# Performance work log

Hardware: AMD Instinct MI355X
Metric: run time of the kernel (lower is better)

The kernel has to match this reference:

```python
import jax, jax.numpy as jnp
import numpy as np

EMBED_DIM = 512
NUM_HEADS = 8
NUM_RULES = 16
HEAD_DIM = EMBED_DIM // NUM_HEADS


def setup_inputs() -> dict:
    key = jax.random.key(0)
    ks = jax.random.split(key, 10)
    B, S, E, H, R, D = 4, 2048, EMBED_DIM, NUM_HEADS, NUM_RULES, HEAD_DIM
    lim_q = 1.0 / np.sqrt(E)
    lim_v = 1.0 / np.sqrt(E)
    return {
        "query": jax.random.normal(ks[0], (B, S, E), jnp.float32),
        "key": jax.random.normal(ks[1], (B, S, E), jnp.float32),
        "value": jax.random.normal(ks[2], (B, S, E), jnp.float32),
        "Wq": jax.random.uniform(ks[3], (E, E), jnp.float32, -lim_q, lim_q),
        "bq": jax.random.uniform(ks[4], (E,), jnp.float32, -lim_q, lim_q),
        "Wv": jax.random.uniform(ks[5], (E * R, E), jnp.float32, -lim_v, lim_v),
        "bv": jax.random.uniform(ks[6], (E * R,), jnp.float32, -lim_v, lim_v),
        "Wo": jax.random.uniform(ks[7], (E, E), jnp.float32, -lim_q, lim_q),
        "bo": jax.random.uniform(ks[8], (E,), jnp.float32, -lim_q, lim_q),
        "rules_keys": 0.02 * jax.random.normal(ks[9], (H, R, D), jnp.float32),
        "rules_widths": jnp.ones((H, R, D), jnp.float32),
    }


def reference(query, key, value, Wq, bq, Wv, bv, Wo, bo, rules_keys, rules_widths):
    B, S, E = query.shape
    H, R, D = NUM_HEADS, NUM_RULES, HEAD_DIM
    scale = D ** -0.5
    # preprocessing_query: Linear + scale, split heads -> (b, h, s, d)
    q = (query @ Wq.T + bq) * scale
    q = q.reshape(B, S, H, D).transpose(0, 2, 1, 3)
    # custom_distance (l1): |q - rule_key| broadcast over rules -> (b, h, s, r, d)
    diff = jnp.abs(q[:, :, :, None, :] - rules_keys[None, :, None, :, :])
    # get_z_values: z = mean_d( -0.5 * (diff / width)^2 ) -> (b, h, s, r)
    z = -0.5 * jnp.mean(jnp.square(diff / rules_widths[None, :, None, :, :]), axis=-1)
    # softmax over rules (last dim), dropout is identity (p=0)
    attn = jax.nn.softmax(z, axis=-1)  # (b, h, s, r)
    # preprocessing_value: Linear(E -> E*R) + scale, 'b s (h d r) -> b s h d r'
    v = (value @ Wv.T + bv) * scale
    v = v.reshape(B, S, H, D, R)
    # Fnn_output = attn * v summed over rules -> (b, s, h, d)
    out = jnp.einsum("bhsr,bshdr->bshd", attn, v)
    # torch: (b,s,h,d).transpose(1,2).contiguous().view(b, -1, h*d)
    out = out.transpose(0, 2, 1, 3).reshape(B, -1, H * D)
    return out @ Wo.T + bo
```

## Files before the change

kernel.cpp:

```cpp
#include <hip/hip_runtime.h>
#include <stdint.h>

#define TOKENS 8192
#define EDIM 512
#define HNUM 8
#define RNUM 16
#define DDIM 64
#define KDIM 512

typedef short v8s __attribute__((ext_vector_type(8)));
typedef float v4f __attribute__((ext_vector_type(4)));

__device__ inline float b2f(unsigned short u) {
    union { unsigned int i; float f; } c; c.i = ((unsigned int)u) << 16; return c.f;
}
__device__ inline unsigned short f2b(float f) {
    union { float f; unsigned int i; } c; c.f = f;
    unsigned int i = c.i + 0x7fffu + ((c.i >> 16) & 1u);
    return (unsigned short)(i >> 16);
}

#define GLD16(dst, src) \
    __builtin_amdgcn_global_load_lds((__attribute__((address_space(1))) void*)(src), \
                                     (__attribute__((address_space(3))) void*)(dst), 16, 0, 0)

__global__ __launch_bounds__(256)
void cvt5(const float* __restrict__ s0, const float* __restrict__ s1,
          const float* __restrict__ s2, const float* __restrict__ s3,
          const float* __restrict__ s4,
          unsigned short* __restrict__ d0, unsigned short* __restrict__ d1,
          unsigned short* __restrict__ d2, unsigned short* __restrict__ d3,
          unsigned short* __restrict__ d4,
          int n0, int n1, int n2, int n3, int n4)
{
    const float* s; unsigned short* d; int n;
    switch (blockIdx.y) {
        case 0: s = s0; d = d0; n = n0; break;
        case 1: s = s1; d = d1; n = n1; break;
        case 2: s = s2; d = d2; n = n2; break;
        case 3: s = s3; d = d3; n = n3; break;
        default: s = s4; d = d4; n = n4; break;
    }
    size_t base = (size_t)blockIdx.x * 2048 + (size_t)threadIdx.x * 8;
    if (base >= (size_t)n) return;
    const float4* sp = (const float4*)(s + base);
    float4 f0 = sp[0], f1 = sp[1];
    v8s o;
    o[0] = (short)f2b(f0.x); o[1] = (short)f2b(f0.y);
    o[2] = (short)f2b(f0.z); o[3] = (short)f2b(f0.w);
    o[4] = (short)f2b(f1.x); o[5] = (short)f2b(f1.y);
    o[6] = (short)f2b(f1.z); o[7] = (short)f2b(f1.w);
    *(v8s*)(d + base) = o;
}

template <int MODE>
__global__ __launch_bounds__(256, 4)
void gemm64(const unsigned short* __restrict__ A,
            const unsigned short* __restrict__ B,
            const float* __restrict__ bias,
            float* __restrict__ outF,
            unsigned short* __restrict__ outH)
{
    __shared__ unsigned short As[64 * 32];
    __shared__ unsigned short Bs[64 * 32];

    const int tid  = threadIdx.x;
    const int w    = tid >> 6;
    const int lane = tid & 63;
    const int quad = lane >> 4;
    const int l16  = lane & 15;
    const int wm   = w >> 1, wn = w & 1;
    const int m0   = blockIdx.x * 64;
    const int n0   = blockIdx.y * 64;

    v4f acc[2][2];
#pragma unroll
    for (int i = 0; i < 2; ++i)
#pragma unroll
        for (int j = 0; j < 2; ++j)
            acc[i][j] = (v4f){0.f, 0.f, 0.f, 0.f};

    for (int kt = 0; kt < KDIM / 32; ++kt) {
        int c = w * 64 + lane;
        const unsigned short* sa = A + (size_t)(m0 + (c >> 2)) * KDIM + kt * 32 + (c & 3) * 8;
        GLD16(&As[w * 512], sa);
        const unsigned short* sb = B + (size_t)(n0 + (c >> 2)) * KDIM + kt * 32 + (c & 3) * 8;
        GLD16(&Bs[w * 512], sb);
        __syncthreads();

        v8s af[2], bf[2];
#pragma unroll
        for (int mt = 0; mt < 2; ++mt)
            af[mt] = *(const v8s*)&As[(wm * 32 + mt * 16 + l16) * 32 + quad * 8];
#pragma unroll
        for (int nt = 0; nt < 2; ++nt)
            bf[nt] = *(const v8s*)&Bs[(wn * 32 + nt * 16 + l16) * 32 + quad * 8];
#pragma unroll
        for (int mt = 0; mt < 2; ++mt)
#pragma unroll
            for (int nt = 0; nt < 2; ++nt)
                acc[mt][nt] = __builtin_amdgcn_mfma_f32_16x16x32_bf16(af[mt], bf[nt], acc[mt][nt], 0, 0, 0);
        __syncthreads();
    }

#pragma unroll
    for (int mt = 0; mt < 2; ++mt)
#pragma unroll
        for (int nt = 0; nt < 2; ++nt) {
            int col = n0 + wn * 32 + nt * 16 + l16;
            float bb = bias[col];
#pragma unroll
            for (int rg = 0; rg < 4; ++rg) {
                int row = m0 + wm * 32 + mt * 16 + quad * 4 + rg;
                float v = acc[mt][nt][rg] + bb;
                if (MODE == 0) outH[(size_t)row * EDIM + col] = f2b(v * 0.125f);
                else           outF[(size_t)row * EDIM + col] = v;
            }
        }
}

__device__ __forceinline__ v8s ldfrag(const unsigned short* base, int r, int g) {
    return *(const v8s*)(base + (r << 6) + ((g ^ (r & 7)) << 3));
}

#define BAR   __builtin_amdgcn_s_barrier()
#define LGKM0 asm volatile("s_waitcnt lgkmcnt(0)" ::: "memory")
#define WAITV(n) asm volatile("s_waitcnt vmcnt(" #n ")" ::: "memory")

#define STAGE_H(ldsArr, bufi, half_, gptr, rowbase, ktv) do { \
    const unsigned short* s_ = (gptr) + (size_t)((rowbase) + (half_) * 128 + (w << 4) + rsub) * KDIM \
                               + (ktv) * 64 + (gsw << 3); \
    GLD16(&ldsArr[bufi][(half_) * 8192 + (w << 10)], s_); \
    GLD16(&ldsArr[bufi][(half_) * 8192 + (w << 10) + 512], s_ + 8 * KDIM); \
} while (0)

#define LDA8(mq_) do { \
    _Pragma("unroll") \
    for (int mi = 0; mi < 4; ++mi) \
        _Pragma("unroll") \
        for (int ks = 0; ks < 2; ++ks) \
            af[mi * 2 + ks] = ldfrag(abase, wm * 64 + (mq_) * 128 + mi * 16 + l16, ks * 4 + quad); \
} while (0)

#define LDB4(nq_, dst) do { \
    _Pragma("unroll") \
    for (int ni = 0; ni < 2; ++ni) \
        _Pragma("unroll") \
        for (int ks = 0; ks < 2; ++ks) \
            dst[ni * 2 + ks] = ldfrag(bbase, wn * 32 + (nq_) * 128 + ni * 16 + l16, ks * 4 + quad); \
} while (0)

#define MFMA16(ai_, bfr) do { \
    _Pragma("unroll") \
    for (int ks = 0; ks < 2; ++ks) \
        _Pragma("unroll") \
        for (int mi = 0; mi < 4; ++mi) \
            _Pragma("unroll") \
            for (int ni = 0; ni < 2; ++ni) \
                acc[ai_][mi][ni] = __builtin_amdgcn_mfma_f32_16x16x32_bf16( \
                    af[mi * 2 + ks], bfr[ni * 2 + ks], acc[ai_][mi][ni], 0, 0, 0); \
} while (0)

__global__ __launch_bounds__(512, 2)
void gemm_v(const unsigned short* __restrict__ A,
            const unsigned short* __restrict__ B,
            const float* __restrict__ bias,
            unsigned short* __restrict__ outH,
            const float* __restrict__ attn)
{
    __shared__ unsigned short As[2][16384];
    __shared__ unsigned short Bs[2][16384];

    const int tid  = threadIdx.x;
    const int w    = tid >> 6;
    const int lane = tid & 63;
    const int quad = lane >> 4;
    const int l16  = lane & 15;
    const int wm   = w >> 2;
    const int wn   = w & 3;
    const int rsub = lane >> 3;
    const int gsw  = (lane & 7) ^ rsub;

    const int c  = blockIdx.x & 7;
    const int j  = blockIdx.x >> 3;
    const int mb = (j & 7) | ((j >> 5) << 3);
    const int nb = (j >> 3) & 3;
    const int m0 = mb << 8;
    const int n0 = (c * 4 + nb) << 8;

    v4f acc[4][4][2];
#pragma unroll
    for (int q = 0; q < 4; ++q)
#pragma unroll
        for (int mi = 0; mi < 4; ++mi)
#pragma unroll
            for (int ni = 0; ni < 2; ++ni)
                acc[q][mi][ni] = (v4f){0.f, 0.f, 0.f, 0.f};

    v8s af[8], bf0[4], bf1[4];

    STAGE_H(As, 0, 0, A, m0, 0);
    STAGE_H(Bs, 0, 0, B, n0, 0);
    STAGE_H(As, 0, 1, A, m0, 0);
    STAGE_H(Bs, 0, 1, B, n0, 0);
    STAGE_H(As, 1, 0, A, m0, 1);
    STAGE_H(Bs, 1, 1, B, n0, 1);
    WAITV(4);
    BAR;

#pragma unroll
    for (int T = 0; T < KDIM / 64; ++T) {
        const unsigned short* abase = &As[T & 1][0];
        const unsigned short* bbase = &Bs[T & 1][0];
        const int bn_ = (T & 1) ^ 1;

        LDA8(0); LDB4(0, bf0);
        if (T + 1 < 8) STAGE_H(As, bn_, 1, A, m0, T + 1);
        BAR; LGKM0;
        __builtin_amdgcn_s_setprio(1); MFMA16(0, bf0); __builtin_amdgcn_s_setprio(0);
        BAR;

        LDB4(1, bf1);
        if (T + 1 < 8) STAGE_H(Bs, bn_, 0, B, n0, T + 1);
        BAR; LGKM0;
        __builtin_amdgcn_s_setprio(1); MFMA16(1, bf1); __builtin_amdgcn_s_setprio(0);
        BAR;

        LDA8(1);
        if (T + 2 < 8) STAGE_H(As, T & 1, 0, A, m0, T + 2);
        BAR; LGKM0;
        __builtin_amdgcn_s_setprio(1); MFMA16(3, bf1); __builtin_amdgcn_s_setprio(0);
        BAR;

        if (T + 2 < 8) STAGE_H(Bs, T & 1, 1, B, n0, T + 2);
        BAR; LGKM0;
        __builtin_amdgcn_s_setprio(1); MFMA16(2, bf0); __builtin_amdgcn_s_setprio(0);
        if (T < 6) { WAITV(4); } else { WAITV(0); }
        BAR;
    }

    unsigned short* Osp = &As[0][0];
    const int h  = m0 >> 10;
    const int d0 = (m0 >> 4) & 63;
#pragma unroll
    for (int mq = 0; mq < 2; ++mq)
#pragma unroll
        for (int nq = 0; nq < 2; ++nq)
#pragma unroll
            for (int mi = 0; mi < 4; ++mi) {
                float4 bias4 = *(const float4*)&bias[m0 + mq * 128 + wm * 64 + mi * 16 + quad * 4];
#pragma unroll
                for (int ni = 0; ni < 2; ++ni) {
                    int tloc  = nq * 128 + wn * 32 + ni * 16 + l16;
                    float4 av = *(const float4*)&attn[(size_t)(n0 + tloc) * (HNUM * RNUM) + h * RNUM + quad * 4];
                    v4f a = acc[mq * 2 + nq][mi][ni];
                    float val = (a[0] + bias4.x) * av.x + (a[1] + bias4.y) * av.y
                              + (a[2] + bias4.z) * av.z + (a[3] + bias4.w) * av.w;
                    val += __shfl_xor(val, 16);
                    val += __shfl_xor(val, 32);
                    if (quad == 0)
                        Osp[tloc * 16 + (mq * 8 + wm * 4 + mi)] = f2b(val * 0.125f);
                }
            }
    __syncthreads();
    {
        int tl = tid >> 1, hf = tid & 1;
        int sg = n0 + tl;
        int g  = (sg >> 11) * 2048 + h * 256 + ((sg & 2047) >> 3);
        int jx = (sg & 7) * 64 + d0 + hf * 8;
        *(v8s*)&outH[(size_t)g * EDIM + jx] = *(const v8s*)&Osp[tl * 16 + hf * 8];
    }
}

#define RST 72
__global__ __launch_bounds__(256)
void rules_softmax(const unsigned short* __restrict__ q,
                   const float* __restrict__ rk,
                   const float* __restrict__ rw,
                   float* __restrict__ attn)
{
    __shared__ float ql[16 * RST];
    __shared__ float rkl[16 * RST];
    __shared__ float iwl[16 * RST];
    const int h   = blockIdx.y;
    const int t0  = blockIdx.x * 16;
    const int tid = threadIdx.x;

#pragma unroll
    for (int i = 0; i < 4; ++i) {
        int jj = tid + i * 256;
        int r = jj >> 6, d = jj & 63;
        rkl[r * RST + d] = rk[h * (RNUM * DDIM) + jj];
        float wv = rw[h * (RNUM * DDIM) + jj];
        iwl[r * RST + d] = 1.0f / (wv * wv);
    }
    {
        int jj = tid * 4;
        int row = jj >> 6, d = jj & 63;
        const unsigned short* src = q + (size_t)(t0 + row) * EDIM + h * DDIM + d;
        unsigned short u0 = src[0], u1 = src[1], u2 = src[2], u3 = src[3];
        ql[row * RST + d + 0] = b2f(u0);
        ql[row * RST + d + 1] = b2f(u1);
        ql[row * RST + d + 2] = b2f(u2);
        ql[row * RST + d + 3] = b2f(u3);
    }
    __syncthreads();

    const int tl = tid >> 4;
    const int r  = tid & 15;
    const float* qrow = &ql[tl * RST];
    const float* krow = &rkl[r * RST];
    const float* wrow = &iwl[r * RST];
    float z = 0.f;
#pragma unroll
    for (int d4 = 0; d4 < 16; ++d4) {
        float4 qv = *(const float4*)&qrow[d4 * 4];
        float4 kv = *(const float4*)&krow[d4 * 4];
        float4 wv = *(const float4*)&wrow[d4 * 4];
        float a0 = qv.x - kv.x; z += a0 * a0 * wv.x;
        float a1 = qv.y - kv.y; z += a1 * a1 * wv.y;
        float a2 = qv.z - kv.z; z += a2 * a2 * wv.z;
        float a3 = qv.w - kv.w; z += a3 * a3 * wv.w;
    }
    z *= (-0.5f / 64.f);
    float mx = z;
#pragma unroll
    for (int s = 1; s < 16; s <<= 1) mx = fmaxf(mx, __shfl_xor(mx, s));
    float e = __expf(z - mx);
    float sum = e;
#pragma unroll
    for (int s = 1; s < 16; s <<= 1) sum += __shfl_xor(sum, s);
    attn[(size_t)(t0 + tl) * (HNUM * RNUM) + h * RNUM + r] = e / sum;
}

extern "C" void kernel_launch(void* const* d_in, const int* in_sizes, int n_in,
                              void* d_out, int out_size, void* d_ws, size_t ws_size,
                              hipStream_t stream) {
    const float* query = (const float*)d_in[0];
    const float* value = (const float*)d_in[2];
    const float* Wq = (const float*)d_in[3];
    const float* bq = (const float*)d_in[4];
    const float* Wv = (const float*)d_in[5];
    const float* bv = (const float*)d_in[6];
    const float* Wo = (const float*)d_in[7];
    const float* bo = (const float*)d_in[8];
    const float* rk = (const float*)d_in[9];
    const float* rw = (const float*)d_in[10];

    char* ws = (char*)d_ws;
    unsigned short* qbf  = (unsigned short*)(ws);
    unsigned short* vbf  = (unsigned short*)(ws + (size_t)( 8 << 20));
    unsigned short* Wqb  = (unsigned short*)(ws + (size_t)(16 << 20));
    unsigned short* Wvb  = (unsigned short*)(ws + (size_t)(17 << 20));
    unsigned short* Wob  = (unsigned short*)(ws + (size_t)(25 << 20));
    unsigned short* out1 = (unsigned short*)(ws + (size_t)(26 << 20));
    unsigned short* qf   = (unsigned short*)(ws + (size_t)(34 << 20));
    float* attn          = (float*)(ws + (size_t)(42 << 20));

    dim3 blk(256);
    cvt5<<<dim3(2048, 5), blk, 0, stream>>>(query, value, Wv, Wq, Wo,
                                            qbf, vbf, Wvb, Wqb, Wob,
                                            TOKENS * EDIM, TOKENS * EDIM, EDIM * RNUM * EDIM,
                                            EDIM * EDIM, EDIM * EDIM);
    gemm64<0><<<dim3(TOKENS / 64, EDIM / 64), blk, 0, stream>>>(qbf, Wqb, bq, nullptr, qf);
    rules_softmax<<<dim3(TOKENS / 16, HNUM), blk, 0, stream>>>(qf, rk, rw, attn);
    gemm_v<<<dim3(1024), dim3(512), 0, stream>>>(Wvb, vbf, bv, out1, attn);
    gemm64<2><<<dim3(TOKENS / 64, EDIM / 64), blk, 0, stream>>>(out1, Wob, bo, (float*)d_out, nullptr);
}
```

Measured before the change: 230.0 us.

## Cut workgroup barriers in the value GEMM main loop from eight to two

Restructures the synchronisation plan of the double-buffered value-projection GEMM. Each K-step used to issue a barrier and an explicit lgkmcnt wait around every one of its four MFMA blocks; now only two barriers are placed, at the points where an LDS buffer half is about to be overwritten by an async global-to-LDS load. The explicit lgkmcnt waits are dropped and the compiler is left to insert LDS-read waits, with compiler memory fences added around the barriers. The aim is to remove barrier stalls and let waves drift so MFMA work overlaps LDS reads and loads. The trade-off is losing the lockstep ping-pong schedule that the s_setprio boosts were built around, which may make MFMA issue less regular.

New measurement: 227.3 us. About the same (-1.2%).

```diff
diff --git a/kernel.cpp b/kernel.cpp
--- a/kernel.cpp
+++ b/kernel.cpp
@@ -123,8 +123,8 @@
     return *(const v8s*)(base + (r << 6) + ((g ^ (r & 7)) << 3));
 }
 
-#define BAR   __builtin_amdgcn_s_barrier()
-#define LGKM0 asm volatile("s_waitcnt lgkmcnt(0)" ::: "memory")
+#define MEMBAR asm volatile("" ::: "memory")
+#define BARX do { MEMBAR; __builtin_amdgcn_s_barrier(); MEMBAR; } while (0)
 #define WAITV(n) asm volatile("s_waitcnt vmcnt(" #n ")" ::: "memory")
 
 #define STAGE_H(ldsArr, bufi, half_, gptr, rowbase, ktv) do { \
@@ -151,6 +151,7 @@
 } while (0)
 
 #define MFMA16(ai_, bfr) do { \
+    __builtin_amdgcn_s_setprio(1); \
     _Pragma("unroll") \
     for (int ks = 0; ks < 2; ++ks) \
         _Pragma("unroll") \
@@ -159,6 +160,7 @@
             for (int ni = 0; ni < 2; ++ni) \
                 acc[ai_][mi][ni] = __builtin_amdgcn_mfma_f32_16x16x32_bf16( \
                     af[mi * 2 + ks], bfr[ni * 2 + ks], acc[ai_][mi][ni], 0, 0, 0); \
+    __builtin_amdgcn_s_setprio(0); \
 } while (0)
 
 __global__ __launch_bounds__(512, 2)
@@ -206,37 +208,29 @@
     STAGE_H(As, 1, 0, A, m0, 1);
     STAGE_H(Bs, 1, 1, B, n0, 1);
     WAITV(4);
-    BAR;
+    BARX;
 
 #pragma unroll
     for (int T = 0; T < KDIM / 64; ++T) {
         const unsigned short* abase = &As[T & 1][0];
         const unsigned short* bbase = &Bs[T & 1][0];
-        const int bn_ = (T & 1) ^ 1;
+        const int ob = (T & 1) ^ 1;
 
         LDA8(0); LDB4(0, bf0);
-        if (T + 1 < 8) STAGE_H(As, bn_, 1, A, m0, T + 1);
-        BAR; LGKM0;
-        __builtin_amdgcn_s_setprio(1); MFMA16(0, bf0); __builtin_amdgcn_s_setprio(0);
-        BAR;
-
+        if (T < 7) STAGE_H(As, ob, 1, A, m0, T + 1);
+        MFMA16(0, bf0);
         LDB4(1, bf1);
-        if (T + 1 < 8) STAGE_H(Bs, bn_, 0, B, n0, T + 1);
-        BAR; LGKM0;
-        __builtin_amdgcn_s_setprio(1); MFMA16(1, bf1); __builtin_amdgcn_s_setprio(0);
-        BAR;
+        if (T < 7) STAGE_H(Bs, ob, 0, B, n0, T + 1);
+        MFMA16(1, bf1);
+        BARX;
 
         LDA8(1);
-        if (T + 2 < 8) STAGE_H(As, T & 1, 0, A, m0, T + 2);
-        BAR; LGKM0;
-        __builtin_amdgcn_s_setprio(1); MFMA16(3, bf1); __builtin_amdgcn_s_setprio(0);
-        BAR;
-
-        if (T + 2 < 8) STAGE_H(Bs, T & 1, 1, B, n0, T + 2);
-        BAR; LGKM0;
-        __builtin_amdgcn_s_setprio(1); MFMA16(2, bf0); __builtin_amdgcn_s_setprio(0);
+        if (T < 6) STAGE_H(As, T & 1, 0, A, m0, T + 2);
+        MFMA16(3, bf1);
+        if (T < 6) STAGE_H(Bs, T & 1, 1, B, n0, T + 2);
+        MFMA16(2, bf0);
         if (T < 6) { WAITV(4); } else { WAITV(0); }
-        BAR;
+        BARX;
     }
 
     unsigned short* Osp = &As[0][0];
```
